# Kernel optimization log

Measured on AMD Instinct MI355X. Metric: run time of the kernel, lower is better.

The kernel has to match this reference:

```python
import jax, jax.numpy as jnp
import numpy as np

B, N, E, H = 2, 2048, 256, 8
D = E // H  # head dim = 32


def setup_inputs() -> dict:
    key = jax.random.key(0)
    ks = jax.random.split(key, 8)
    query_bbox = jax.random.uniform(ks[0], (B, N, 4), dtype=jnp.float32)
    query_feat = jax.random.normal(ks[1], (B, N, E), dtype=jnp.float32)
    s = 1.0 / np.sqrt(E)
    in_proj_w = jax.random.uniform(ks[2], (3 * E, E), minval=-s, maxval=s, dtype=jnp.float32)
    in_proj_b = jax.random.uniform(ks[3], (3 * E,), minval=-s, maxval=s, dtype=jnp.float32)
    out_proj_w = jax.random.uniform(ks[4], (E, E), minval=-s, maxval=s, dtype=jnp.float32)
    out_proj_b = jnp.zeros((E,), dtype=jnp.float32)
    # init_weights(): gen_tau weight zeroed, bias ~ U(0, 2)
    tau_w = jnp.zeros((H, E), dtype=jnp.float32)
    tau_b = jax.random.uniform(ks[5], (H,), minval=0.0, maxval=2.0, dtype=jnp.float32)
    return {
        "query_bbox": query_bbox,
        "query_feat": query_feat,
        "in_proj_w": in_proj_w,
        "in_proj_b": in_proj_b,
        "out_proj_w": out_proj_w,
        "out_proj_b": out_proj_b,
        "tau_w": tau_w,
        "tau_b": tau_b,
    }


def reference(query_bbox, query_feat, in_proj_w, in_proj_b, out_proj_w, out_proj_b, tau_w, tau_b):
    # pairwise center distances, negated; computed under no_grad in torch
    centers = query_bbox[..., :2]                                  # [B,N,2]
    diff = centers[:, :, None, :] - centers[:, None, :, :]         # [B,N,N,2]
    dist = -jnp.sqrt(jnp.sum(diff * diff, axis=-1))                # [B,N,N]
    dist = jax.lax.stop_gradient(dist)

    # per-head tau from query features
    tau = query_feat @ tau_w.T + tau_b                             # [B,N,H]
    tau = jnp.transpose(tau, (0, 2, 1))                            # [B,H,N]
    attn_mask = dist[:, None, :, :] * tau[..., None]               # [B,H,N,N]

    # multi-head self-attention (q = k = v = query_feat)
    qkv = query_feat @ in_proj_w.T + in_proj_b                     # [B,N,3E]
    q, k, v = jnp.split(qkv, 3, axis=-1)
    def heads(x):
        return jnp.transpose(x.reshape(B, N, H, D), (0, 2, 1, 3))  # [B,H,N,D]
    q, k, v = heads(q), heads(k), heads(v)

    scores = jnp.einsum("bhid,bhjd->bhij", q, k) / jnp.sqrt(jnp.float32(D))
    scores = scores + attn_mask
    attn = jax.nn.softmax(scores, axis=-1)                         # [B,H,N,N]
    o = jnp.einsum("bhij,bhjd->bhid", attn, v)                     # [B,H,N,D]
    o = jnp.transpose(o, (0, 2, 1, 3)).reshape(B, N, E)
    out = o @ out_proj_w.T + out_proj_b

    # mmcv MultiheadAttention adds the identity (residual); dropout in eval = id
    return query_feat + out
```

## Files before the change

### kernel.cpp

```cpp
#include <hip/hip_runtime.h>
#include <math.h>

#define BB 2
#define NN 2048
#define EE 256
#define HH 8
#define DD 32

typedef __attribute__((ext_vector_type(8))) short short8;
typedef __attribute__((ext_vector_type(4))) float f32x4;

__device__ inline unsigned short f2bf(float f) {
  union { float f; unsigned int u; } a; a.f = f;
  unsigned int r = a.u + 0x7FFFu + ((a.u >> 16) & 1u);
  return (unsigned short)(r >> 16);
}
__device__ inline float bf2f(short s) {
  union { unsigned int u; float f; } a;
  a.u = ((unsigned int)(unsigned short)s) << 16;
  return a.f;
}

__global__ __launch_bounds__(256) void cast_w_kernel(const float* __restrict__ in_w,
                                                     const float* __restrict__ out_w,
                                                     unsigned short* __restrict__ in_wb,
                                                     unsigned short* __restrict__ out_wb) {
  int i = blockIdx.x * 256 + threadIdx.x;
  float4 v;
  unsigned short* dst;
  if (i < 49152) {
    v = ((const float4*)in_w)[i];
    dst = in_wb + (size_t)i * 4;
  } else {
    v = ((const float4*)out_w)[i - 49152];
    dst = out_wb + (size_t)(i - 49152) * 4;
  }
  ushort4 u;
  u.x = f2bf(v.x); u.y = f2bf(v.y); u.z = f2bf(v.z); u.w = f2bf(v.w);
  *(ushort4*)dst = u;
}

__global__ __launch_bounds__(256) void tau_cxy_kernel(const float* __restrict__ feat,
                                                      const float* __restrict__ tau_w,
                                                      const float* __restrict__ tau_b,
                                                      const float* __restrict__ bbox,
                                                      float* __restrict__ tau2,
                                                      float2* __restrict__ cxy,
                                                      unsigned short* __restrict__ featb) {
  int idx = blockIdx.x * 256 + threadIdx.x;
  int row = idx >> 3, h = idx & 7;
  const float4* f = (const float4*)(feat + (size_t)row * EE);
  const float4* w = (const float4*)(tau_w + (size_t)h * EE);
  float s = 0.f;
#pragma unroll 8
  for (int e = 0; e < EE / 4; ++e) {
    float4 a = f[e], b4 = w[e];
    s = fmaf(a.x, b4.x, s);
    s = fmaf(a.y, b4.y, s);
    s = fmaf(a.z, b4.z, s);
    s = fmaf(a.w, b4.w, s);
    if ((e >> 3) == h) {
      ushort4 u;
      u.x = f2bf(a.x); u.y = f2bf(a.y); u.z = f2bf(a.z); u.w = f2bf(a.w);
      *(ushort4*)(featb + (size_t)row * EE + e * 4) = u;
    }
  }
  tau2[idx] = (s + tau_b[h]) * 1.4426950408889634f;
  if (h == 0) {
    float2 c;
    c.x = bbox[(size_t)row * 4 + 0];
    c.y = bbox[(size_t)row * 4 + 1];
    cxy[row] = c;
  }
}

__global__ __launch_bounds__(256) void dist_kernel(const float2* __restrict__ cxy,
                                                   unsigned short* __restrict__ nds) {
  int bq = blockIdx.x;
  int b = bq >> 7, qt = bq & 127;
  int tid = threadIdx.x;
  int w = tid >> 6, lane = tid & 63;
  int q15 = lane & 15, g = lane >> 4;
  int jt = blockIdx.y * 4 + w;

  float2 ci = cxy[b * NN + qt * 16 + q15];
  const float2* cb = cxy + b * NN + jt * 64;

  float nd[16];
#pragma unroll
  for (int t = 0; t < 4; ++t) {
    float4 c01 = *(const float4*)(cb + t * 16 + g * 4);
    float4 c23 = *(const float4*)(cb + t * 16 + g * 4 + 2);
    float cx[4] = {c01.x, c01.z, c23.x, c23.z};
    float cy[4] = {c01.y, c01.w, c23.y, c23.w};
#pragma unroll
    for (int r = 0; r < 4; ++r) {
      float dx = ci.x - cx[r], dy = ci.y - cy[r];
      nd[t * 4 + r] = -__builtin_amdgcn_sqrtf(fmaf(dy, dy, dx * dx));
    }
  }
  unsigned int u[8];
#pragma unroll
  for (int i = 0; i < 8; ++i)
    asm("v_cvt_pk_bf16_f32 %0, %1, %2" : "=v"(u[i]) : "v"(nd[2 * i]), "v"(nd[2 * i + 1]));
  unsigned short* dst = nds + ((size_t)(b * 128 + qt) * 32 + jt) * 1024 + lane * 16;
  *(uint4*)dst = make_uint4(u[0], u[1], u[2], u[3]);
  *(uint4*)(dst + 8) = make_uint4(u[4], u[5], u[6], u[7]);
}

template <int MODE>
__global__ __launch_bounds__(256) void gemm_mfma_kernel(const unsigned short* __restrict__ Ab,
                                                        const unsigned short* __restrict__ Wb,
                                                        const float* __restrict__ bias,
                                                        const float* __restrict__ resid,
                                                        float* __restrict__ Cf,
                                                        unsigned short* __restrict__ qb,
                                                        unsigned short* __restrict__ kh,
                                                        unsigned short* __restrict__ vpi) {
  int tid = threadIdx.x;
  int wv = tid >> 6, lane = tid & 63;
  int p = lane & 15, g = lane >> 4;
  int mW = blockIdx.y * 64 + wv * 16;
  int nB = blockIdx.x * 64;

  const unsigned short* ap = Ab + (size_t)(mW + p) * 256 + g * 8;
  const unsigned short* wp = Wb + (size_t)(nB + p) * 256 + g * 8;

  f32x4 acc[4] = {{0.f, 0.f, 0.f, 0.f}, {0.f, 0.f, 0.f, 0.f},
                  {0.f, 0.f, 0.f, 0.f}, {0.f, 0.f, 0.f, 0.f}};
#pragma unroll
  for (int kk = 0; kk < 8; ++kk) {
    short8 af = *(const short8*)(ap + kk * 32);
#pragma unroll
    for (int t = 0; t < 4; ++t) {
      short8 wf = *(const short8*)(wp + (size_t)t * 16 * 256 + kk * 32);
      acc[t] = __builtin_amdgcn_mfma_f32_16x16x32_bf16(af, wf, acc[t], 0, 0, 0);
    }
  }

#pragma unroll
  for (int t = 0; t < 4; ++t) {
    int n = nB + t * 16 + p;
    float bn = bias[n];
#pragma unroll
    for (int r = 0; r < 4; ++r) {
      int m = mW + g * 4 + r;
      float v = acc[t][r] + bn;
      if (MODE == 1) {
        Cf[(size_t)m * 256 + n] = v + resid[(size_t)m * 256 + n];
      } else {
        int b = m >> 11, tok = m & 2047;
        if (n < 256) {
          qb[(size_t)m * 256 + n] = f2bf(v * 0.25506659272582955f);
        } else if (n < 512) {
          int h = (n - 256) >> 5, d = n & 31;
          kh[((size_t)(b * 8 + h) * NN + tok) * 32 + d] = f2bf(v);
        } else {
          int h = (n - 512) >> 5, d = n & 31;
          int cp = ((tok & 15) << 1) | ((tok >> 4) & 1);
          vpi[(((size_t)(b * 8 + h) * 64 + (tok >> 5)) * 32 + d) * 32 + cp] = f2bf(v);
        }
      }
    }
  }
}

__global__ __launch_bounds__(256) void attn_kernel(const unsigned short* __restrict__ qb,
                                                   const unsigned short* __restrict__ kh,
                                                   const unsigned short* __restrict__ vpi,
                                                   const unsigned short* __restrict__ nds,
                                                   const float* __restrict__ tau2,
                                                   unsigned short* __restrict__ ob) {
  __shared__ float accT[4][32][17];
  __shared__ float lT[4][16];
  __shared__ float linv[16];

  int bh = blockIdx.x;
  int b = bh >> 3, h = bh & 7;
  int qtb = blockIdx.y;
  int tid = threadIdx.x;
  int w = tid >> 6;
  int lane = tid & 63;
  int q15 = lane & 15, g = lane >> 4;
  int rowq = b * NN + qtb * 16 + q15;

  short8 qf = *(const short8*)(qb + (size_t)rowq * 256 + h * 32 + g * 8);
  float t2 = tau2[(size_t)rowq * HH + h];

  float l = 0.f;
  f32x4 acc0 = {0.f, 0.f, 0.f, 0.f}, acc1 = {0.f, 0.f, 0.f, 0.f};

  const unsigned short* kb = kh + (size_t)bh * NN * 32 + q15 * 32 + g * 8;
  const unsigned short* vb = vpi + (size_t)bh * NN * 32 + q15 * 32 + g * 8;
  const unsigned short* ndb = nds + (size_t)(b * 128 + qtb) * 32 * 1024 + lane * 16;

  int j0base = w * 512;

  short8 kf[2][4];
  short8 vf[2][2];

#pragma unroll
  for (int t = 0; t < 4; ++t)
    kf[0][t] = *(const short8*)(kb + (size_t)(j0base + t * 16) * 32);

#pragma unroll
  for (int tt = 0; tt < 8; ++tt) {
    const int cur = tt & 1, nxt = cur ^ 1;
    const int j0 = j0base + tt * 64;
    const int jt = j0 >> 6;
    if (tt < 7) {
#pragma unroll
      for (int t = 0; t < 4; ++t)
        kf[nxt][t] = *(const short8*)(kb + (size_t)(j0 + 64 + t * 16) * 32);
    }
#pragma unroll
    for (int t2i = 0; t2i < 2; ++t2i)
#pragma unroll
      for (int dh = 0; dh < 2; ++dh)
        vf[t2i][dh] = *(const short8*)(vb + (size_t)((j0 >> 5) + t2i) * 1024 + dh * 512);
    short8 n0 = *(const short8*)(ndb + (size_t)jt * 1024);
    short8 n1 = *(const short8*)(ndb + (size_t)jt * 1024 + 8);
    f32x4 st[4];
#pragma unroll
    for (int t = 0; t < 4; ++t)
      st[t] = __builtin_amdgcn_mfma_f32_16x16x32_bf16(kf[cur][t], qf, (f32x4){0.f, 0.f, 0.f, 0.f}, 0, 0, 0);
    float p[16], lsum = 0.f;
#pragma unroll
    for (int i = 0; i < 16; ++i) {
      float ndf = bf2f(i < 8 ? n0[i] : n1[i - 8]);
      float e = fminf(fmaf(ndf, t2, st[i >> 2][i & 3]), 30.f);
      p[i] = __builtin_amdgcn_exp2f(e);
      lsum += p[i];
    }
    l += lsum;
    union { short8 v; unsigned int u[4]; } pf[2];
#pragma unroll
    for (int t2i = 0; t2i < 2; ++t2i)
#pragma unroll
      for (int wq = 0; wq < 4; ++wq) {
        float lo = p[t2i * 8 + wq];
        float hi = p[t2i * 8 + 4 + wq];
        asm("v_cvt_pk_bf16_f32 %0, %1, %2" : "=v"(pf[t2i].u[wq]) : "v"(lo), "v"(hi));
      }
    acc0 = __builtin_amdgcn_mfma_f32_16x16x32_bf16(vf[0][0], pf[0].v, acc0, 0, 0, 0);
    acc1 = __builtin_amdgcn_mfma_f32_16x16x32_bf16(vf[0][1], pf[0].v, acc1, 0, 0, 0);
    acc0 = __builtin_amdgcn_mfma_f32_16x16x32_bf16(vf[1][0], pf[1].v, acc0, 0, 0, 0);
    acc1 = __builtin_amdgcn_mfma_f32_16x16x32_bf16(vf[1][1], pf[1].v, acc1, 0, 0, 0);
  }

  l += __shfl_xor(l, 16);
  l += __shfl_xor(l, 32);

#pragma unroll
  for (int r = 0; r < 4; ++r) {
    accT[w][g * 4 + r][q15] = acc0[r];
    accT[w][16 + g * 4 + r][q15] = acc1[r];
  }
  if (g == 0) lT[w][q15] = l;
  __syncthreads();

  if (tid < 16) {
    float L = lT[0][tid] + lT[1][tid] + lT[2][tid] + lT[3][tid];
    linv[tid] = 1.f / fmaxf(L, 1e-30f);
  }
  __syncthreads();

#pragma unroll
  for (int ii = 0; ii < 2; ++ii) {
    int i = tid + ii * 256;
    int q = i >> 5, d = i & 31;
    float ov = (accT[0][d][q] + accT[1][d][q] + accT[2][d][q] + accT[3][d][q]) * linv[q];
    ob[((size_t)b * NN + qtb * 16 + q) * EE + h * 32 + d] = f2bf(ov);
  }
}

extern "C" void kernel_launch(void* const* d_in, const int* in_sizes, int n_in,
                              void* d_out, int out_size, void* d_ws, size_t ws_size,
                              hipStream_t stream) {
  const float* bbox  = (const float*)d_in[0];
  const float* feat  = (const float*)d_in[1];
  const float* in_w  = (const float*)d_in[2];
  const float* in_b  = (const float*)d_in[3];
  const float* out_w = (const float*)d_in[4];
  const float* out_b = (const float*)d_in[5];
  const float* tau_w = (const float*)d_in[6];
  const float* tau_b = (const float*)d_in[7];
  float* out = (float*)d_out;

  unsigned short* ob     = (unsigned short*)d_ws;
  unsigned short* featb  = ob + 1048576;
  unsigned short* qb     = featb + 1048576;
  unsigned short* kh     = qb + 1048576;
  unsigned short* vpi    = kh + 1048576;
  unsigned short* in_wb  = vpi + 1048576;
  unsigned short* out_wb = in_wb + 196608;
  float* tau2 = (float*)(out_wb + 65536);
  float2* cxy = (float2*)(tau2 + 32768);
  unsigned short* nds = (unsigned short*)(cxy + 4096);

  cast_w_kernel<<<dim3(256), 256, 0, stream>>>(in_w, out_w, in_wb, out_wb);
  tau_cxy_kernel<<<dim3(128), 256, 0, stream>>>(feat, tau_w, tau_b, bbox, tau2, cxy, featb);
  dist_kernel<<<dim3(BB * 128, 8), 256, 0, stream>>>(cxy, nds);
  gemm_mfma_kernel<0><<<dim3(12, 64), 256, 0, stream>>>(featb, in_wb, in_b, nullptr, nullptr,
                                                        qb, kh, vpi);
  attn_kernel<<<dim3(BB * HH, NN / 16), 256, 0, stream>>>(qb, kh, vpi, nds, tau2, ob);
  gemm_mfma_kernel<1><<<dim3(4, 64), 256, 0, stream>>>(ob, out_wb, out_b, feat, out,
                                                       nullptr, nullptr, nullptr);
}
```

Before: 98.59 us.

## Merge prep kernels into one launch and double-buffer V and distance loads

Folds the weight cast, tau/feature cast and distance kernels into a single prep kernel that picks its role by block index. The distance part now reads centers straight from bbox instead of going through an intermediate cxy buffer, which removes two launches and one dependency. In the attention loop, V fragments and distance values are now prefetched one tile ahead alongside K, to hide load latency at the cost of more registers. The strided float2 bbox reads are less efficient than the old packed cxy loads.

```diff
diff --git a/kernel.cpp b/kernel.cpp
--- a/kernel.cpp
+++ b/kernel.cpp
@@ -21,91 +21,85 @@
   return a.f;
 }
 
-__global__ __launch_bounds__(256) void cast_w_kernel(const float* __restrict__ in_w,
-                                                     const float* __restrict__ out_w,
-                                                     unsigned short* __restrict__ in_wb,
-                                                     unsigned short* __restrict__ out_wb) {
-  int i = blockIdx.x * 256 + threadIdx.x;
-  float4 v;
-  unsigned short* dst;
-  if (i < 49152) {
-    v = ((const float4*)in_w)[i];
-    dst = in_wb + (size_t)i * 4;
+__global__ __launch_bounds__(256) void prep_kernel(const float* __restrict__ bbox,
+                                                   const float* __restrict__ feat,
+                                                   const float* __restrict__ in_w,
+                                                   const float* __restrict__ out_w,
+                                                   const float* __restrict__ tau_w,
+                                                   const float* __restrict__ tau_b,
+                                                   unsigned short* __restrict__ in_wb,
+                                                   unsigned short* __restrict__ out_wb,
+                                                   float* __restrict__ tau2,
+                                                   unsigned short* __restrict__ featb,
+                                                   unsigned short* __restrict__ nds) {
+  int blk = blockIdx.x;
+  int tid = threadIdx.x;
+  if (blk < 256) {
+    int i = blk * 256 + tid;
+    float4 v;
+    unsigned short* dst;
+    if (i < 49152) {
+      v = ((const float4*)in_w)[i];
+      dst = in_wb + (size_t)i * 4;
+    } else {
+      v = ((const float4*)out_w)[i - 49152];
+      dst = out_wb + (size_t)(i - 49152) * 4;
+    }
+    ushort4 u;
+    u.x = f2bf(v.x); u.y = f2bf(v.y); u.z = f2bf(v.z); u.w = f2bf(v.w);
+    *(ushort4*)dst = u;
+  } else if (blk < 384) {
+    int idx = (blk - 256) * 256 + tid;
+    int row = idx >> 3, h = idx & 7;
+    const float4* f = (const float4*)(feat + (size_t)row * EE);
+    const float4* w = (const float4*)(tau_w + (size_t)h * EE);
+    float s = 0.f;
+#pragma unroll 8
+    for (int e = 0; e < EE / 4; ++e) {
+      float4 a = f[e], b4 = w[e];
+      s = fmaf(a.x, b4.x, s);
+      s = fmaf(a.y, b4.y, s);
+      s = fmaf(a.z, b4.z, s);
+      s = fmaf(a.w, b4.w, s);
+      if ((e >> 3) == h) {
+        ushort4 u;
+        u.x = f2bf(a.x); u.y = f2bf(a.y); u.z = f2bf(a.z); u.w = f2bf(a.w);
+        *(ushort4*)(featb + (size_t)row * EE + e * 4) = u;
+      }
+    }
+    tau2[idx] = (s + tau_b[h]) * 1.4426950408889634f;
   } else {
-    v = ((const float4*)out_w)[i - 49152];
-    dst = out_wb + (size_t)(i - 49152) * 4;
-  }
-  ushort4 u;
-  u.x = f2bf(v.x); u.y = f2bf(v.y); u.z = f2bf(v.z); u.w = f2bf(v.w);
-  *(ushort4*)dst = u;
-}
-
-__global__ __launch_bounds__(256) void tau_cxy_kernel(const float* __restrict__ feat,
-                                                      const float* __restrict__ tau_w,
-                                                      const float* __restrict__ tau_b,
-                                                      const float* __restrict__ bbox,
-                                                      float* __restrict__ tau2,
-                                                      float2* __restrict__ cxy,
-                                                      unsigned short* __restrict__ featb) {
-  int idx = blockIdx.x * 256 + threadIdx.x;
-  int row = idx >> 3, h = idx & 7;
-  const float4* f = (const float4*)(feat + (size_t)row * EE);
-  const float4* w = (const float4*)(tau_w + (size_t)h * EE);
-  float s = 0.f;
-#pragma unroll 8
-  for (int e = 0; e < EE / 4; ++e) {
-    float4 a = f[e], b4 = w[e];
-    s = fmaf(a.x, b4.x, s);
-    s = fmaf(a.y, b4.y, s);
-    s = fmaf(a.z, b4.z, s);
-    s = fmaf(a.w, b4.w, s);
-    if ((e >> 3) == h) {
-      ushort4 u;
-      u.x = f2bf(a.x); u.y = f2bf(a.y); u.z = f2bf(a.z); u.w = f2bf(a.w);
-      *(ushort4*)(featb + (size_t)row * EE + e * 4) = u;
-    }
-  }
-  tau2[idx] = (s + tau_b[h]) * 1.4426950408889634f;
-  if (h == 0) {
-    float2 c;
-    c.x = bbox[(size_t)row * 4 + 0];
-    c.y = bbox[(size_t)row * 4 + 1];
-    cxy[row] = c;
-  }
-}
-
-__global__ __launch_bounds__(256) void dist_kernel(const float2* __restrict__ cxy,
-                                                   unsigned short* __restrict__ nds) {
-  int bq = blockIdx.x;
-  int b = bq >> 7, qt = bq & 127;
-  int tid = threadIdx.x;
-  int w = tid >> 6, lane = tid & 63;
-  int q15 = lane & 15, g = lane >> 4;
-  int jt = blockIdx.y * 4 + w;
-
-  float2 ci = cxy[b * NN + qt * 16 + q15];
-  const float2* cb = cxy + b * NN + jt * 64;
-
-  float nd[16];
-#pragma unroll
-  for (int t = 0; t < 4; ++t) {
-    float4 c01 = *(const float4*)(cb + t * 16 + g * 4);
-    float4 c23 = *(const float4*)(cb + t * 16 + g * 4 + 2);
-    float cx[4] = {c01.x, c01.z, c23.x, c23.z};
-    float cy[4] = {c01.y, c01.w, c23.y, c23.w};
-#pragma unroll
-    for (int r = 0; r < 4; ++r) {
-      float dx = ci.x - cx[r], dy = ci.y - cy[r];
-      nd[t * 4 + r] = -__builtin_amdgcn_sqrtf(fmaf(dy, dy, dx * dx));
-    }
-  }
-  unsigned int u[8];
-#pragma unroll
-  for (int i = 0; i < 8; ++i)
-    asm("v_cvt_pk_bf16_f32 %0, %1, %2" : "=v"(u[i]) : "v"(nd[2 * i]), "v"(nd[2 * i + 1]));
-  unsigned short* dst = nds + ((size_t)(b * 128 + qt) * 32 + jt) * 1024 + lane * 16;
-  *(uint4*)dst = make_uint4(u[0], u[1], u[2], u[3]);
-  *(uint4*)(dst + 8) = make_uint4(u[4], u[5], u[6], u[7]);
+    int blk2 = blk - 384;
+    int bq = blk2 >> 3;
+    int yy = blk2 & 7;
+    int b = bq >> 7, qt = bq & 127;
+    int w = tid >> 6, lane = tid & 63;
+    int q15 = lane & 15, g = lane >> 4;
+    int jt = yy * 4 + w;
+
+    const float* bi = bbox + (size_t)(b * NN + qt * 16 + q15) * 4;
+    float cix = bi[0], ciy = bi[1];
+    const float* bj = bbox + (size_t)(b * NN + jt * 64) * 4;
+
+    float nd[16];
+#pragma unroll
+    for (int t = 0; t < 4; ++t) {
+#pragma unroll
+      for (int r = 0; r < 4; ++r) {
+        int j = t * 16 + g * 4 + r;
+        float2 cj = *(const float2*)(bj + (size_t)j * 4);
+        float dx = cix - cj.x, dy = ciy - cj.y;
+        nd[t * 4 + r] = -__builtin_amdgcn_sqrtf(fmaf(dy, dy, dx * dx));
+      }
+    }
+    unsigned int u[8];
+#pragma unroll
+    for (int i = 0; i < 8; ++i)
+      asm("v_cvt_pk_bf16_f32 %0, %1, %2" : "=v"(u[i]) : "v"(nd[2 * i]), "v"(nd[2 * i + 1]));
+    unsigned short* dst = nds + ((size_t)(b * 128 + qt) * 32 + jt) * 1024 + lane * 16;
+    *(uint4*)dst = make_uint4(u[0], u[1], u[2], u[3]);
+    *(uint4*)(dst + 8) = make_uint4(u[4], u[5], u[6], u[7]);
+  }
 }
 
 template <int MODE>
@@ -192,34 +186,42 @@
 
   const unsigned short* kb = kh + (size_t)bh * NN * 32 + q15 * 32 + g * 8;
   const unsigned short* vb = vpi + (size_t)bh * NN * 32 + q15 * 32 + g * 8;
-  const unsigned short* ndb = nds + (size_t)(b * 128 + qtb) * 32 * 1024 + lane * 16;
+  const unsigned short* ndb = nds + (size_t)(b * 128 + qtb) * 32768 + lane * 16;
 
   int j0base = w * 512;
 
   short8 kf[2][4];
-  short8 vf[2][2];
+  short8 vf[2][2][2];
+  short8 nf[2][2];
 
 #pragma unroll
   for (int t = 0; t < 4; ++t)
     kf[0][t] = *(const short8*)(kb + (size_t)(j0base + t * 16) * 32);
+#pragma unroll
+  for (int t2i = 0; t2i < 2; ++t2i)
+#pragma unroll
+    for (int dh = 0; dh < 2; ++dh)
+      vf[0][t2i][dh] = *(const short8*)(vb + (size_t)((j0base >> 5) + t2i) * 1024 + dh * 512);
+  nf[0][0] = *(const short8*)(ndb + (size_t)(j0base >> 6) * 1024);
+  nf[0][1] = *(const short8*)(ndb + (size_t)(j0base >> 6) * 1024 + 8);
 
 #pragma unroll
   for (int tt = 0; tt < 8; ++tt) {
     const int cur = tt & 1, nxt = cur ^ 1;
     const int j0 = j0base + tt * 64;
-    const int jt = j0 >> 6;
     if (tt < 7) {
+      const int j1 = j0 + 64;
 #pragma unroll
       for (int t = 0; t < 4; ++t)
-        kf[nxt][t] = *(const short8*)(kb + (size_t)(j0 + 64 + t * 16) * 32);
-    }
-#pragma unroll
-    for (int t2i = 0; t2i < 2; ++t2i)
-#pragma unroll
-      for (int dh = 0; dh < 2; ++dh)
-        vf[t2i][dh] = *(const short8*)(vb + (size_t)((j0 >> 5) + t2i) * 1024 + dh * 512);
-    short8 n0 = *(const short8*)(ndb + (size_t)jt * 1024);
-    short8 n1 = *(const short8*)(ndb + (size_t)jt * 1024 + 8);
+        kf[nxt][t] = *(const short8*)(kb + (size_t)(j1 + t * 16) * 32);
+#pragma unroll
+      for (int t2i = 0; t2i < 2; ++t2i)
+#pragma unroll
+        for (int dh = 0; dh < 2; ++dh)
+          vf[nxt][t2i][dh] = *(const short8*)(vb + (size_t)((j1 >> 5) + t2i) * 1024 + dh * 512);
+      nf[nxt][0] = *(const short8*)(ndb + (size_t)(j1 >> 6) * 1024);
+      nf[nxt][1] = *(const short8*)(ndb + (size_t)(j1 >> 6) * 1024 + 8);
+    }
     f32x4 st[4];
 #pragma unroll
     for (int t = 0; t < 4; ++t)
@@ -227,7 +229,7 @@
     float p[16], lsum = 0.f;
 #pragma unroll
     for (int i = 0; i < 16; ++i) {
-      float ndf = bf2f(i < 8 ? n0[i] : n1[i - 8]);
+      float ndf = bf2f(i < 8 ? nf[cur][0][i] : nf[cur][1][i - 8]);
       float e = fminf(fmaf(ndf, t2, st[i >> 2][i & 3]), 30.f);
       p[i] = __builtin_amdgcn_exp2f(e);
       lsum += p[i];
@@ -238,14 +240,13 @@
     for (int t2i = 0; t2i < 2; ++t2i)
 #pragma unroll
       for (int wq = 0; wq < 4; ++wq) {
-        float lo = p[t2i * 8 + wq];
-        float hi = p[t2i * 8 + 4 + wq];
-        asm("v_cvt_pk_bf16_f32 %0, %1, %2" : "=v"(pf[t2i].u[wq]) : "v"(lo), "v"(hi));
+        asm("v_cvt_pk_bf16_f32 %0, %1, %2"
+            : "=v"(pf[t2i].u[wq]) : "v"(p[t2i * 8 + wq]), "v"(p[t2i * 8 + 4 + wq]));
       }
-    acc0 = __builtin_amdgcn_mfma_f32_16x16x32_bf16(vf[0][0], pf[0].v, acc0, 0, 0, 0);
-    acc1 = __builtin_amdgcn_mfma_f32_16x16x32_bf16(vf[0][1], pf[0].v, acc1, 0, 0, 0);
-    acc0 = __builtin_amdgcn_mfma_f32_16x16x32_bf16(vf[1][0], pf[1].v, acc0, 0, 0, 0);
-    acc1 = __builtin_amdgcn_mfma_f32_16x16x32_bf16(vf[1][1], pf[1].v, acc1, 0, 0, 0);
+    acc0 = __builtin_amdgcn_mfma_f32_16x16x32_bf16(vf[cur][0][0], pf[0].v, acc0, 0, 0, 0);
+    acc1 = __builtin_amdgcn_mfma_f32_16x16x32_bf16(vf[cur][0][1], pf[0].v, acc1, 0, 0, 0);
+    acc0 = __builtin_amdgcn_mfma_f32_16x16x32_bf16(vf[cur][1][0], pf[1].v, acc0, 0, 0, 0);
+    acc1 = __builtin_amdgcn_mfma_f32_16x16x32_bf16(vf[cur][1][1], pf[1].v, acc1, 0, 0, 0);
   }
 
   l += __shfl_xor(l, 16);
@@ -295,12 +296,10 @@
   unsigned short* in_wb  = vpi + 1048576;
   unsigned short* out_wb = in_wb + 196608;
   float* tau2 = (float*)(out_wb + 65536);
-  float2* cxy = (float2*)(tau2 + 32768);
-  unsigned short* nds = (unsigned short*)(cxy + 4096);
-
-  cast_w_kernel<<<dim3(256), 256, 0, stream>>>(in_w, out_w, in_wb, out_wb);
-  tau_cxy_kernel<<<dim3(128), 256, 0, stream>>>(feat, tau_w, tau_b, bbox, tau2, cxy, featb);
-  dist_kernel<<<dim3(BB * 128, 8), 256, 0, stream>>>(cxy, nds);
+  unsigned short* nds = (unsigned short*)(tau2 + 32768);
+
+  prep_kernel<<<dim3(2432), 256, 0, stream>>>(bbox, feat, in_w, out_w, tau_w, tau_b,
+                                              in_wb, out_wb, tau2, featb, nds);
   gemm_mfma_kernel<0><<<dim3(12, 64), 256, 0, stream>>>(featb, in_wb, in_b, nullptr, nullptr,
                                                         qb, kh, vpi);
   attn_kernel<<<dim3(BB * HH, NN / 16), 256, 0, stream>>>(qb, kh, vpi, nds, tau2, ob);
```

Result: faster. 90.28 us (median of 2 runs) (-8.4%).
